# Kernel tuning notes

Measured on AMD Instinct MI355X. Metric: run time of the kernel, lower is better.

Reference implementation:

```python
import jax, jax.numpy as jnp
import numpy as np

TEMP = 0.07
BASE_TEMP = 0.07
EPS = 1e-8


def setup_inputs() -> dict:
    key = jax.random.key(0)
    features = jax.random.normal(key, (4096, 2, 128), dtype=jnp.float32)
    return {"features": features}


def reference(features):
    B, V, D = features.shape  # bsz, n_views, dim
    # torch.cat(torch.unbind(features, dim=1), dim=0): view-major ordering
    cf = jnp.swapaxes(features, 0, 1).reshape(V * B, D)  # [N, D], N = V*B
    # cosine similarity = normalize rows then GEMM (same math as broadcasted CosineSimilarity)
    n = cf / jnp.maximum(jnp.linalg.norm(cf, axis=-1, keepdims=True), EPS)
    logits = jnp.matmul(n, n.T) / TEMP  # [N, N]
    N = V * B
    logits_mask = 1.0 - jnp.eye(N, dtype=logits.dtype)  # zero out self-contrast
    # SimCLR mask: eye(B) tiled over (anchor_count, contrast_count), minus diagonal
    pos_mask = jnp.tile(jnp.eye(B, dtype=logits.dtype), (V, V)) * logits_mask
    exp_logits = jnp.exp(logits) * logits_mask
    log_prob = logits - jnp.log(exp_logits.sum(axis=1, keepdims=True))
    mean_log_prob_pos = (pos_mask * log_prob).sum(axis=1) / pos_mask.sum(axis=1)
    loss = -(TEMP / BASE_TEMP) * mean_log_prob_pos
    return loss.reshape(V, B).mean()
```

## Files before the change

kernel.cpp:

```cpp
#include <hip/hip_runtime.h>
#include <hip/hip_bf16.h>
#include <math.h>


constexpr int   Bsz   = 4096;
constexpr int   Nrows = 8192;
constexpr int   Dd    = 128;
constexpr float TEMPf = 0.07f;
constexpr float EPSN  = 1e-8f;
constexpr float SCALE = 1.4426950408889634f / 0.07f;
constexpr float LN2   = 0.6931471805599453f;

constexpr int CHUNKS     = 32;
constexpr int CHUNK_COLS = Nrows / CHUNKS;
constexpr int TILES      = CHUNK_COLS / 32;
constexpr int ROWS_BLK   = 256;
constexpr int YG         = Nrows / ROWS_BLK;
constexpr int PREPBLKS   = Bsz / 4;

typedef __attribute__((ext_vector_type(8)))  short bf16x8;
typedef __attribute__((ext_vector_type(16))) float floatx16;


constexpr size_t OFF_PART = 0x200000;
constexpr size_t OFF_SPOS = 0x300000;

__device__ __forceinline__ void gld_lds16(const void* g, void* l) {
    __builtin_amdgcn_global_load_lds(
        (const __attribute__((address_space(1))) void*)g,
        (__attribute__((address_space(3))) void*)l, 16, 0, 0);
}

__global__ void prep_k(const float* __restrict__ f,
                       char* __restrict__ nF,
                       float* __restrict__ sposPart,
                       float* __restrict__ out) {
    __shared__ float sred[4];
    int tid  = threadIdx.x;
    int wid  = tid >> 6;
    int lane = tid & 63;
    int b    = blockIdx.x * 4 + wid;
    if (blockIdx.x == 0 && tid == 0) out[0] = 0.f;

    const float* s0 = f + (size_t)(b * 2) * Dd;
    float2 x = *(const float2*)(s0 + lane * 2);
    float2 y = *(const float2*)(s0 + Dd + lane * 2);
    float ss0 = x.x * x.x + x.y * x.y;
    float ss1 = y.x * y.x + y.y * y.y;
    float dt  = x.x * y.x + x.y * y.y;
    #pragma unroll
    for (int off = 32; off; off >>= 1) {
        ss0 += __shfl_xor(ss0, off);
        ss1 += __shfl_xor(ss1, off);
        dt  += __shfl_xor(dt,  off);
    }
    float inv0 = 1.0f / fmaxf(sqrtf(ss0), EPSN);
    float inv1 = 1.0f / fmaxf(sqrtf(ss1), EPSN);

    size_t poff = (size_t)(lane >> 3) * 1024 + ((lane >> 2) & 1) * 512
                + (lane & 3) * 4;

    __hip_bfloat162 h;
    h.x = __float2bfloat16(x.x * inv0);
    h.y = __float2bfloat16(x.y * inv0);
    *(__hip_bfloat162*)(nF + (size_t)(b >> 5) * 8192 + (b & 31) * 16 + poff) = h;
    int r1 = Bsz + b;
    h.x = __float2bfloat16(y.x * inv1);
    h.y = __float2bfloat16(y.y * inv1);
    *(__hip_bfloat162*)(nF + (size_t)(r1 >> 5) * 8192 + (r1 & 31) * 16 + poff) = h;

    if (lane == 0) sred[wid] = dt * inv0 * inv1 / TEMPf;
    __syncthreads();
    if (tid == 0) sposPart[blockIdx.x] = sred[0] + sred[1] + sred[2] + sred[3];
}

__global__ __launch_bounds__(256, 4)
void main_k(const char* __restrict__ nF, float* __restrict__ partial) {
    __shared__ char  bufs[2][8192];
    __shared__ float colred[4][256];
    const int tid  = threadIdx.x;
    const int wid  = tid >> 6;
    const int lane = tid & 63;
    const int lo   = lane & 31;
    const int hi   = lane >> 5;
    const int gy   = blockIdx.y;
    const int rbase = gy * ROWS_BLK + wid * 64;
    const int cbase = blockIdx.x * CHUNK_COLS;
    const int cg0   = cbase >> 5;

    bf16x8 afrag[2][8];
    #pragma unroll
    for (int s = 0; s < 2; s++) {
        const char* ag = nF + (size_t)((rbase + s * 32) >> 5) * 8192 + lane * 16;
        #pragma unroll
        for (int kc = 0; kc < 8; kc++)
            afrag[s][kc] = *(const bf16x8*)(ag + kc * 1024);
    }

    {
        const char* g0 = nF + (size_t)cg0 * 8192;
        int kc = wid * 2;
        gld_lds16(g0 + kc * 1024 + lane * 16,       &bufs[0][kc * 1024]);
        gld_lds16(g0 + (kc + 1) * 1024 + lane * 16, &bufs[0][(kc + 1) * 1024]);
    }

    floatx16 zero = {};

    #pragma unroll 1
    for (int t = 0; t < TILES; t++) {
        __syncthreads();
        if (t + 1 < TILES) {
            const char* gn = nF + (size_t)(cg0 + t + 1) * 8192;
            char* dst = bufs[(t + 1) & 1];
            int kc = wid * 2;
            gld_lds16(gn + kc * 1024 + lane * 16,       dst + kc * 1024);
            gld_lds16(gn + (kc + 1) * 1024 + lane * 16, dst + (kc + 1) * 1024);
        }

        const char* buf = bufs[t & 1];
        floatx16 acc0 = zero, acc1 = zero;
        #pragma unroll
        for (int kc = 0; kc < 8; kc++) {
            bf16x8 bf = *(const bf16x8*)&buf[kc * 1024 + lane * 16];
            acc0 = __builtin_amdgcn_mfma_f32_32x32x16_bf16(afrag[0][kc], bf, acc0, 0, 0, 0);
            acc1 = __builtin_amdgcn_mfma_f32_32x32x16_bf16(afrag[1][kc], bf, acc1, 0, 0, 0);
        }

        const int cb32 = cbase + t * 32;
        float cs = 0.f;
        #pragma unroll
        for (int s = 0; s < 2; s++) {
            const floatx16& acc = s ? acc1 : acc0;
            if (cb32 == rbase + s * 32) {
                #pragma unroll
                for (int r = 0; r < 16; r++) {
                    float e = __builtin_amdgcn_exp2f(acc[r] * SCALE);
                    if (lo == ((r & 3) + 8 * (r >> 2) + 4 * hi)) e = 0.f;
                    cs += e;
                }
            } else {
                #pragma unroll
                for (int r = 0; r < 16; r++)
                    cs += __builtin_amdgcn_exp2f(acc[r] * SCALE);
            }
        }
        cs += __shfl_xor(cs, 32);
        if (hi == 0) colred[wid][t * 32 + lo] = cs;
    }

    __syncthreads();
    float v = colred[0][tid] + colred[1][tid] + colred[2][tid] + colred[3][tid];
    partial[(size_t)gy * Nrows + cbase + tid] = v;
}

__global__ __launch_bounds__(256)
void final_k(const float* __restrict__ partial, const float* __restrict__ sposPart,
             float* __restrict__ out) {
    __shared__ float red[4];
    int tid = threadIdx.x;
    int r = blockIdx.x * 256 + tid;
    float se = 0.f;
    #pragma unroll
    for (int p = 0; p < YG; p++) se += partial[(size_t)p * Nrows + r];
    float acc = __builtin_amdgcn_logf(se) * LN2;
    if (tid < 32) acc -= 2.f * sposPart[blockIdx.x * 32 + tid];
    #pragma unroll
    for (int off = 32; off; off >>= 1) acc += __shfl_xor(acc, off);
    if ((tid & 63) == 0) red[tid >> 6] = acc;
    __syncthreads();
    if (tid == 0)
        atomicAdd(out, (red[0] + red[1] + red[2] + red[3]) / (float)Nrows);
}

extern "C" void kernel_launch(void* const* d_in, const int* in_sizes, int n_in,
                              void* d_out, int out_size, void* d_ws, size_t ws_size,
                              hipStream_t stream) {
    const float* f = (const float*)d_in[0];
    char* ws = (char*)d_ws;
    char* nF        = ws;
    float* partial  = (float*)(ws + OFF_PART);
    float* sposPart = (float*)(ws + OFF_SPOS);

    prep_k<<<PREPBLKS, 256, 0, stream>>>(f, nF, sposPart, (float*)d_out);
    dim3 grid(CHUNKS, YG);
    main_k<<<grid, 256, 0, stream>>>(nF, partial);
    final_k<<<Nrows / 256, 256, 0, stream>>>(partial, sposPart, (float*)d_out);
}
```

Before: 79.80 us.

## Preload whole column chunk to LDS and write per-wave partial sums

The main kernel now loads all eight 32-column tiles of its chunk into shared memory (64 KB) once, then loops without per-tile barriers or double buffering. The block-level column reduction through shared memory is removed: each wave writes its own partial column sums to global memory, and the final kernel reduces over four times as many slices. This removes per-iteration synchronisation, but the larger LDS footprint drops occupancy (launch bounds 4 to 2) and the partial-sum buffer and final-kernel reads grow fourfold.

New measurement: 87.55 us. +9.7%, slower.

```diff
diff --git a/kernel.cpp b/kernel.cpp
--- a/kernel.cpp
+++ b/kernel.cpp
@@ -16,6 +16,7 @@
 constexpr int TILES      = CHUNK_COLS / 32;
 constexpr int ROWS_BLK   = 256;
 constexpr int YG         = Nrows / ROWS_BLK;
+constexpr int WSLICES    = YG * 4;
 constexpr int PREPBLKS   = Bsz / 4;
 
 typedef __attribute__((ext_vector_type(8)))  short bf16x8;
@@ -23,7 +24,7 @@
 
 
 constexpr size_t OFF_PART = 0x200000;
-constexpr size_t OFF_SPOS = 0x300000;
+constexpr size_t OFF_SPOS = 0x600000;
 
 __device__ __forceinline__ void gld_lds16(const void* g, void* l) {
     __builtin_amdgcn_global_load_lds(
@@ -74,10 +75,9 @@
     if (tid == 0) sposPart[blockIdx.x] = sred[0] + sred[1] + sred[2] + sred[3];
 }
 
-__global__ __launch_bounds__(256, 4)
-void main_k(const char* __restrict__ nF, float* __restrict__ partial) {
-    __shared__ char  bufs[2][8192];
-    __shared__ float colred[4][256];
+__global__ __launch_bounds__(256, 2)
+void main_k(const char* __restrict__ nF, float* __restrict__ partialW) {
+    __shared__ char buf[TILES][8192];
     const int tid  = threadIdx.x;
     const int wid  = tid >> 6;
     const int lane = tid & 63;
@@ -88,6 +88,18 @@
     const int cbase = blockIdx.x * CHUNK_COLS;
     const int cg0   = cbase >> 5;
 
+    {
+        const char* gsrc = nF + (size_t)cg0 * 8192;
+        #pragma unroll
+        for (int g = 0; g < 2; g++) {
+            int t = wid * 2 + g;
+            #pragma unroll
+            for (int kc = 0; kc < 8; kc++)
+                gld_lds16(gsrc + (size_t)t * 8192 + kc * 1024 + lane * 16,
+                          &buf[t][kc * 1024]);
+        }
+    }
+
     bf16x8 afrag[2][8];
     #pragma unroll
     for (int s = 0; s < 2; s++) {
@@ -97,31 +109,17 @@
             afrag[s][kc] = *(const bf16x8*)(ag + kc * 1024);
     }
 
-    {
-        const char* g0 = nF + (size_t)cg0 * 8192;
-        int kc = wid * 2;
-        gld_lds16(g0 + kc * 1024 + lane * 16,       &bufs[0][kc * 1024]);
-        gld_lds16(g0 + (kc + 1) * 1024 + lane * 16, &bufs[0][(kc + 1) * 1024]);
-    }
+    __syncthreads();
 
     floatx16 zero = {};
+    float* wrow = partialW + (size_t)(gy * 4 + wid) * Nrows + cbase;
 
     #pragma unroll 1
     for (int t = 0; t < TILES; t++) {
-        __syncthreads();
-        if (t + 1 < TILES) {
-            const char* gn = nF + (size_t)(cg0 + t + 1) * 8192;
-            char* dst = bufs[(t + 1) & 1];
-            int kc = wid * 2;
-            gld_lds16(gn + kc * 1024 + lane * 16,       dst + kc * 1024);
-            gld_lds16(gn + (kc + 1) * 1024 + lane * 16, dst + (kc + 1) * 1024);
-        }
-
-        const char* buf = bufs[t & 1];
         floatx16 acc0 = zero, acc1 = zero;
         #pragma unroll
         for (int kc = 0; kc < 8; kc++) {
-            bf16x8 bf = *(const bf16x8*)&buf[kc * 1024 + lane * 16];
+            bf16x8 bf = *(const bf16x8*)&buf[t][kc * 1024 + lane * 16];
             acc0 = __builtin_amdgcn_mfma_f32_32x32x16_bf16(afrag[0][kc], bf, acc0, 0, 0, 0);
             acc1 = __builtin_amdgcn_mfma_f32_32x32x16_bf16(afrag[1][kc], bf, acc1, 0, 0, 0);
         }
@@ -145,23 +143,19 @@
             }
         }
         cs += __shfl_xor(cs, 32);
-        if (hi == 0) colred[wid][t * 32 + lo] = cs;
+        if (hi == 0) wrow[t * 32 + lo] = cs;
     }
-
-    __syncthreads();
-    float v = colred[0][tid] + colred[1][tid] + colred[2][tid] + colred[3][tid];
-    partial[(size_t)gy * Nrows + cbase + tid] = v;
 }
 
 __global__ __launch_bounds__(256)
-void final_k(const float* __restrict__ partial, const float* __restrict__ sposPart,
+void final_k(const float* __restrict__ partialW, const float* __restrict__ sposPart,
              float* __restrict__ out) {
     __shared__ float red[4];
     int tid = threadIdx.x;
     int r = blockIdx.x * 256 + tid;
     float se = 0.f;
-    #pragma unroll
-    for (int p = 0; p < YG; p++) se += partial[(size_t)p * Nrows + r];
+    #pragma unroll 4
+    for (int p = 0; p < WSLICES; p++) se += partialW[(size_t)p * Nrows + r];
     float acc = __builtin_amdgcn_logf(se) * LN2;
     if (tid < 32) acc -= 2.f * sposPart[blockIdx.x * 32 + tid];
     #pragma unroll
@@ -178,11 +172,11 @@
     const float* f = (const float*)d_in[0];
     char* ws = (char*)d_ws;
     char* nF        = ws;
-    float* partial  = (float*)(ws + OFF_PART);
+    float* partialW = (float*)(ws + OFF_PART);
     float* sposPart = (float*)(ws + OFF_SPOS);
 
     prep_k<<<PREPBLKS, 256, 0, stream>>>(f, nF, sposPart, (float*)d_out);
     dim3 grid(CHUNKS, YG);
-    main_k<<<grid, 256, 0, stream>>>(nF, partial);
-    final_k<<<Nrows / 256, 256, 0, stream>>>(partial, sposPart, (float*)d_out);
+    main_k<<<grid, 256, 0, stream>>>(nF, partialW);
+    final_k<<<Nrows / 256, 256, 0, stream>>>(partialW, sposPart, (float*)d_out);
 }
```
